# Kernel optimization log

Measured on AMD Instinct MI355X. Metric: run time of the kernel, lower is better.

Reference implementation:

```python
import jax, jax.numpy as jnp
import numpy as np

MARGIN = 0.2
EPS = 1e-5
NEG_SENTINEL = -1e9


def _cos_sim(a, b):
    a = a / jnp.linalg.norm(a, axis=-1, keepdims=True)
    b = b / jnp.linalg.norm(b, axis=-1, keepdims=True)
    return a @ b.T  # [B, B]


def _row_losses(sm, labels):
    # sm: [B, B] similarity matrix; one loop body of the original, vectorized over rows i.
    diag = jnp.diagonal(sm)                      # pos_pair_ (scalar per row)
    pos_valid = diag < (1.0 - EPS)               # pos_pair_[pos_pair_ < 1-eps]
    neg_mask = labels[None, :] != labels[:, None]
    # neg_pair_[neg_pair_ + margin > min(pos_pair_)] ; min of a scalar is itself
    hard = neg_mask & ((sm + MARGIN) > diag[:, None])
    has_neg = jnp.any(hard, axis=1)
    neg_max = jnp.max(jnp.where(hard, sm, NEG_SENTINEL), axis=1)  # max(neg_pair)
    valid = pos_valid & has_neg
    pos_loss = jnp.maximum(0.2 * diag * diag - 0.7 * diag + 0.5, 0.0)
    neg_loss = jnp.maximum(0.9 * neg_max * neg_max - 0.4 * neg_max + 0.03, 0.0)
    return jnp.sum(jnp.where(valid, pos_loss + neg_loss, 0.0))


def setup_inputs() -> dict:
    key = jax.random.key(0)
    k1, k2 = jax.random.split(key)
    B, D = 8192, 256
    audio_embeds = jax.random.normal(k1, (B, D), dtype=jnp.float32)
    text_embeds = jax.random.normal(k2, (B, D), dtype=jnp.float32)
    labels = jnp.arange(B, dtype=jnp.int64)
    return {"audio_embeds": audio_embeds, "text_embeds": text_embeds, "labels": labels}


def reference(audio_embeds, text_embeds, labels):
    scores = _cos_sim(audio_embeds, text_embeds)  # [B, B]
    B = scores.shape[0]
    total = _row_losses(scores, labels) + _row_losses(scores.T, labels)
    return total / B
```

## Files before the change

kernel.cpp:

```cpp
#include <hip/hip_runtime.h>
#include <stdint.h>

#define BM 128
#define BN 128
#define KD 256

typedef __attribute__((ext_vector_type(4))) float f32x4;
typedef __attribute__((ext_vector_type(4))) int   i32x4;
typedef __attribute__((ext_vector_type(8))) int   i32x8;

__device__ __forceinline__ float fmax4(f32x4 v) {
  return fmaxf(fmaxf(v[0], v[1]), fmaxf(v[2], v[3]));
}

__global__ __launch_bounds__(256) void norm_kernel(
    const float* __restrict__ a, const float* __restrict__ b,
    unsigned int* __restrict__ an, unsigned int* __restrict__ bn,
    float* __restrict__ diag, float* __restrict__ out, int D) {
  if (blockIdx.x == 0 && threadIdx.x == 0) out[0] = 0.f;
  const int row = blockIdx.x * 4 + (threadIdx.x >> 6);
  const int l = threadIdx.x & 63;
  const float4 av = ((const float4*)(a + (size_t)row * D))[l];
  const float4 bv = ((const float4*)(b + (size_t)row * D))[l];
  float ssa = av.x*av.x + av.y*av.y + av.z*av.z + av.w*av.w;
  float ssb = bv.x*bv.x + bv.y*bv.y + bv.z*bv.z + bv.w*bv.w;
  float dot = av.x*bv.x + av.y*bv.y + av.z*bv.z + av.w*bv.w;
  for (int off = 1; off < 64; off <<= 1) {
    ssa += __shfl_xor(ssa, off, 64);
    ssb += __shfl_xor(ssb, off, 64);
    dot += __shfl_xor(dot, off, 64);
  }
  const float inva = 1.0f / sqrtf(ssa);
  const float invb = 1.0f / sqrtf(ssb);
  if (l == 0) diag[row] = dot * inva * invb;
  int pa = 0, pb = 0;
  pa = __builtin_amdgcn_cvt_pk_fp8_f32(av.x * inva, av.y * inva, pa, 0);
  pa = __builtin_amdgcn_cvt_pk_fp8_f32(av.z * inva, av.w * inva, pa, 1);
  pb = __builtin_amdgcn_cvt_pk_fp8_f32(bv.x * invb, bv.y * invb, pb, 0);
  pb = __builtin_amdgcn_cvt_pk_fp8_f32(bv.z * invb, bv.w * invb, pb, 1);
  an[(size_t)row * (D / 4) + l] = (unsigned int)pa;
  bn[(size_t)row * (D / 4) + l] = (unsigned int)pb;
}

__global__ __launch_bounds__(256, 2) void gemm_max_kernel(
    const unsigned char* __restrict__ an, const unsigned char* __restrict__ bn,
    const int* __restrict__ labels,
    float* __restrict__ row_part, float* __restrict__ col_part, int B) {
  __shared__ __align__(16) unsigned char sA[BM * KD];
  __shared__ __align__(16) unsigned char sB[BN * KD];
  __shared__ float lds_col[2][BN];

  const int tid  = threadIdx.x;
  const int lane = tid & 63;
  const int w    = tid >> 6;
  const int wm   = w >> 1, wn = w & 1;
  const int tj   = blockIdx.x & 63;
  const int ti   = blockIdx.x >> 6;

  const int sr = lane >> 4;
  const int sc = lane & 15;

  const int fr = lane & 15;
  const int hi = lane >> 4;
  const int p0 = ((2 * hi)     ^ (fr & 7)) * 16;
  const int p1 = ((2 * hi + 1) ^ (fr & 7)) * 16;

  #pragma unroll
  for (int pass = 0; pass < 8; ++pass) {
    const int r0  = pass * 16 + w * 4;
    const int row = r0 + sr;
    const int g = ((sc & 7) ^ (row & 7)) | (sc & 8);
    const unsigned char* ga = an + (size_t)(ti * BM + row) * KD + g * 16;
    const unsigned char* gb = bn + (size_t)(tj * BN + row) * KD + g * 16;
    __builtin_amdgcn_global_load_lds(
        (const __attribute__((address_space(1))) void*)ga,
        (__attribute__((address_space(3))) void*)(sA + r0 * KD + lane * 16), 16, 0, 0);
    __builtin_amdgcn_global_load_lds(
        (const __attribute__((address_space(1))) void*)gb,
        (__attribute__((address_space(3))) void*)(sB + r0 * KD + lane * 16), 16, 0, 0);
  }
  __syncthreads();

  f32x4 acc[4][4];
  #pragma unroll
  for (int mt = 0; mt < 4; ++mt)
    #pragma unroll
    for (int nt = 0; nt < 4; ++nt)
      acc[mt][nt] = (f32x4){0.f, 0.f, 0.f, 0.f};

  const int SC = 0x7F7F7F7F;

  #pragma unroll
  for (int it = 0; it < 2; ++it) {
    i32x8 bf[4];
    #pragma unroll
    for (int nt = 0; nt < 4; ++nt) {
      const unsigned char* rb = sB + (wn * 64 + nt * 16 + fr) * KD + it * 128;
      i32x4 blo = *(const i32x4*)(rb + p0), bhi = *(const i32x4*)(rb + p1);
      bf[nt] = __builtin_shufflevector(blo, bhi, 0, 1, 2, 3, 4, 5, 6, 7);
    }
    #pragma unroll
    for (int mt = 0; mt < 4; ++mt) {
      const unsigned char* ra = sA + (wm * 64 + mt * 16 + fr) * KD + it * 128;
      i32x4 alo = *(const i32x4*)(ra + p0), ahi = *(const i32x4*)(ra + p1);
      i32x8 af = __builtin_shufflevector(alo, ahi, 0, 1, 2, 3, 4, 5, 6, 7);
      #pragma unroll
      for (int nt = 0; nt < 4; ++nt)
        acc[mt][nt] = __builtin_amdgcn_mfma_scale_f32_16x16x128_f8f6f4(
            af, bf[nt], acc[mt][nt], 0, 0, 0, SC, 0, SC);
    }
  }
  __syncthreads();

  int li[4][4], labc[4];
  #pragma unroll
  for (int mt = 0; mt < 4; ++mt)
    #pragma unroll
    for (int r = 0; r < 4; ++r)
      li[mt][r] = labels[ti * BM + wm * 64 + mt * 16 + hi * 4 + r];
  #pragma unroll
  for (int nt = 0; nt < 4; ++nt)
    labc[nt] = labels[tj * BN + wn * 64 + nt * 16 + fr];

  float rp[4][4];
  float cp[4] = {-1e9f, -1e9f, -1e9f, -1e9f};
  #pragma unroll
  for (int mt = 0; mt < 4; ++mt)
    #pragma unroll
    for (int r = 0; r < 4; ++r) {
      const int l0 = li[mt][r];
      float rm = -1e9f;
      #pragma unroll
      for (int nt = 0; nt < 4; ++nt) {
        const float vm = (l0 != labc[nt]) ? acc[mt][nt][r] : -1e9f;
        rm = fmaxf(rm, vm);
        cp[nt] = fmaxf(cp[nt], vm);
      }
      rp[mt][r] = rm;
    }

  float* red = (float*)sA;
  const int s = wn * 16 + fr;
  #pragma unroll
  for (int mt = 0; mt < 4; ++mt)
    #pragma unroll
    for (int r = 0; r < 4; ++r) {
      const int i = wm * 64 + mt * 16 + hi * 4 + r;
      red[i * 32 + (((s >> 2) ^ (i & 7)) << 2) + (s & 3)] = rp[mt][r];
    }

  #pragma unroll
  for (int nt = 0; nt < 4; ++nt) {
    float c = cp[nt];
    c = fmaxf(c, __shfl_xor(c, 16, 64));
    c = fmaxf(c, __shfl_xor(c, 32, 64));
    if (hi == 0) lds_col[wm][wn * 64 + nt * 16 + fr] = c;
  }
  __syncthreads();

  if (tid < BM) {
    const int key = tid & 7;
    const f32x4* rr = (const f32x4*)(red + tid * 32);
    f32x4 m4 = rr[0 ^ key];
    #pragma unroll
    for (int k = 1; k < 8; ++k) {
      f32x4 v = rr[k ^ key];
      m4[0] = fmaxf(m4[0], v[0]); m4[1] = fmaxf(m4[1], v[1]);
      m4[2] = fmaxf(m4[2], v[2]); m4[3] = fmaxf(m4[3], v[3]);
    }
    row_part[(size_t)tj * B + ti * BM + tid] = fmax4(m4);
  } else if (tid < BM + BN) {
    const int t2 = tid - BM;
    col_part[(size_t)ti * B + tj * BN + t2] =
        fmaxf(lds_col[0][t2], lds_col[1][t2]);
  }
}

__global__ __launch_bounds__(256) void finalize_kernel(
    const float* __restrict__ row_part, const float* __restrict__ col_part,
    const float* __restrict__ diag, int B, int T, float* __restrict__ out) {
  const int v = blockIdx.x * 256 + threadIdx.x;
  const bool isrow = v < B;
  const int i = isrow ? v : v - B;
  const float* part = isrow ? row_part : col_part;
  float m = -1e9f;
  for (int t = 0; t < T; ++t) m = fmaxf(m, part[(size_t)t * B + i]);
  const float d = diag[i];
  float loss = 0.f;
  if ((d < 1.0f - 1e-5f) && (m + 0.2f > d)) {
    loss = fmaxf(0.2f * d * d - 0.7f * d + 0.5f, 0.f) +
           fmaxf(0.9f * m * m - 0.4f * m + 0.03f, 0.f);
  }
  for (int off = 1; off < 64; off <<= 1) loss += __shfl_xor(loss, off, 64);
  __shared__ float ssum[4];
  if ((threadIdx.x & 63) == 0) ssum[threadIdx.x >> 6] = loss;
  __syncthreads();
  if (threadIdx.x == 0)
    atomicAdd(out, (ssum[0] + ssum[1] + ssum[2] + ssum[3]) / (float)B);
}

extern "C" void kernel_launch(void* const* d_in, const int* in_sizes, int n_in,
                              void* d_out, int out_size, void* d_ws, size_t ws_size,
                              hipStream_t stream) {
  const float* a      = (const float*)d_in[0];
  const float* b      = (const float*)d_in[1];
  const int*   labels = (const int*)d_in[2];
  const int B = in_sizes[2];
  const int D = in_sizes[0] / B;
  const int T = B / BM;

  char* ws = (char*)d_ws;
  unsigned char* an = (unsigned char*)ws;
  unsigned char* bn = (unsigned char*)(ws + (size_t)B * D);
  float* diag     = (float*)(ws + (size_t)2 * B * D);
  float* row_part = diag + B;
  float* col_part = row_part + (size_t)T * B;

  norm_kernel<<<B / 4, 256, 0, stream>>>(a, b, (unsigned int*)an,
                                         (unsigned int*)bn, diag,
                                         (float*)d_out, D);

  gemm_max_kernel<<<(B / BM) * (B / BN), 256, 0, stream>>>(
      an, bn, labels, row_part, col_part, B);

  finalize_kernel<<<(2 * B) / 256, 256, 0, stream>>>(
      row_part, col_part, diag, B, T, (float*)d_out);
}
```

Before: 123.5 us.

## Make GEMM blocks loop over 16 A tiles with double-buffered LDS prefetch

Each GEMM block now keeps one B column tile resident in LDS and loops over 16 A row tiles. It prefetches the next A tile into a second LDS buffer while computing the current one, with 512 threads arranged as 2x4 waves. The launch drops from 4096 blocks to 256, cutting repeated B loads and per-block setup. Row maxima are reduced with wave shuffles and written straight to global memory per wave column instead of through an LDS reduction. This enlarges the row partial buffer fourfold and makes the finalize pass read many more partials per row, while column partials shrink to four per column.

```diff
diff --git a/kernel.cpp b/kernel.cpp
--- a/kernel.cpp
+++ b/kernel.cpp
@@ -8,10 +8,6 @@
 typedef __attribute__((ext_vector_type(4))) float f32x4;
 typedef __attribute__((ext_vector_type(4))) int   i32x4;
 typedef __attribute__((ext_vector_type(8))) int   i32x8;
-
-__device__ __forceinline__ float fmax4(f32x4 v) {
-  return fmaxf(fmaxf(v[0], v[1]), fmaxf(v[2], v[3]));
-}
 
 __global__ __launch_bounds__(256) void norm_kernel(
     const float* __restrict__ a, const float* __restrict__ b,
@@ -42,20 +38,20 @@
   bn[(size_t)row * (D / 4) + l] = (unsigned int)pb;
 }
 
-__global__ __launch_bounds__(256, 2) void gemm_max_kernel(
+__global__ __launch_bounds__(512, 2) void gemm_max_kernel(
     const unsigned char* __restrict__ an, const unsigned char* __restrict__ bn,
     const int* __restrict__ labels,
     float* __restrict__ row_part, float* __restrict__ col_part, int B) {
-  __shared__ __align__(16) unsigned char sA[BM * KD];
+  __shared__ __align__(16) unsigned char sA[2 * BM * KD];
   __shared__ __align__(16) unsigned char sB[BN * KD];
   __shared__ float lds_col[2][BN];
 
   const int tid  = threadIdx.x;
   const int lane = tid & 63;
   const int w    = tid >> 6;
-  const int wm   = w >> 1, wn = w & 1;
+  const int wm   = w >> 2, wn = w & 3;
+  const int g0   = blockIdx.x >> 6;
   const int tj   = blockIdx.x & 63;
-  const int ti   = blockIdx.x >> 6;
 
   const int sr = lane >> 4;
   const int sc = lane & 15;
@@ -66,123 +62,135 @@
   const int p1 = ((2 * hi + 1) ^ (fr & 7)) * 16;
 
   #pragma unroll
-  for (int pass = 0; pass < 8; ++pass) {
-    const int r0  = pass * 16 + w * 4;
+  for (int pass = 0; pass < 4; ++pass) {
+    const int r0  = pass * 32 + w * 4;
     const int row = r0 + sr;
     const int g = ((sc & 7) ^ (row & 7)) | (sc & 8);
-    const unsigned char* ga = an + (size_t)(ti * BM + row) * KD + g * 16;
     const unsigned char* gb = bn + (size_t)(tj * BN + row) * KD + g * 16;
+    const unsigned char* ga = an + (size_t)(g0 * BM + row) * KD + g * 16;
+    __builtin_amdgcn_global_load_lds(
+        (const __attribute__((address_space(1))) void*)gb,
+        (__attribute__((address_space(3))) void*)(sB + r0 * KD + lane * 16), 16, 0, 0);
     __builtin_amdgcn_global_load_lds(
         (const __attribute__((address_space(1))) void*)ga,
         (__attribute__((address_space(3))) void*)(sA + r0 * KD + lane * 16), 16, 0, 0);
-    __builtin_amdgcn_global_load_lds(
-        (const __attribute__((address_space(1))) void*)gb,
-        (__attribute__((address_space(3))) void*)(sB + r0 * KD + lane * 16), 16, 0, 0);
   }
   __syncthreads();
 
-  f32x4 acc[4][4];
+  int labc[2];
+  labc[0] = labels[tj * BN + wn * 32 + fr];
+  labc[1] = labels[tj * BN + wn * 32 + 16 + fr];
+
+  const int SC = 0x7F7F7F7F;
+  float cp[2] = {-1e9f, -1e9f};
+  int bsel = 0;
+
+  for (int k = 0; k < 16; ++k) {
+    const int ti = g0 + 4 * k;
+
+    if (k < 15) {
+      const int tin = g0 + 4 * (k + 1);
+      #pragma unroll
+      for (int pass = 0; pass < 4; ++pass) {
+        const int r0  = pass * 32 + w * 4;
+        const int row = r0 + sr;
+        const int g = ((sc & 7) ^ (row & 7)) | (sc & 8);
+        const unsigned char* ga = an + (size_t)(tin * BM + row) * KD + g * 16;
+        __builtin_amdgcn_global_load_lds(
+            (const __attribute__((address_space(1))) void*)ga,
+            (__attribute__((address_space(3))) void*)
+                (sA + (bsel ^ 1) * (BM * KD) + r0 * KD + lane * 16), 16, 0, 0);
+      }
+    }
+
+    f32x4 acc[4][2];
+    #pragma unroll
+    for (int mt = 0; mt < 4; ++mt) {
+      acc[mt][0] = (f32x4){0.f, 0.f, 0.f, 0.f};
+      acc[mt][1] = (f32x4){0.f, 0.f, 0.f, 0.f};
+    }
+    const unsigned char* Ab = sA + bsel * (BM * KD);
+    #pragma unroll
+    for (int it = 0; it < 2; ++it) {
+      i32x8 bf[2];
+      #pragma unroll
+      for (int nt = 0; nt < 2; ++nt) {
+        const unsigned char* rb = sB + (wn * 32 + nt * 16 + fr) * KD + it * 128;
+        bf[nt] = __builtin_shufflevector(*(const i32x4*)(rb + p0),
+                                         *(const i32x4*)(rb + p1),
+                                         0, 1, 2, 3, 4, 5, 6, 7);
+      }
+      #pragma unroll
+      for (int mt = 0; mt < 4; ++mt) {
+        const unsigned char* ra = Ab + (wm * 64 + mt * 16 + fr) * KD + it * 128;
+        i32x8 af = __builtin_shufflevector(*(const i32x4*)(ra + p0),
+                                           *(const i32x4*)(ra + p1),
+                                           0, 1, 2, 3, 4, 5, 6, 7);
+        acc[mt][0] = __builtin_amdgcn_mfma_scale_f32_16x16x128_f8f6f4(
+            af, bf[0], acc[mt][0], 0, 0, 0, SC, 0, SC);
+        acc[mt][1] = __builtin_amdgcn_mfma_scale_f32_16x16x128_f8f6f4(
+            af, bf[1], acc[mt][1], 0, 0, 0, SC, 0, SC);
+      }
+    }
+
+    int li[4][4];
+    #pragma unroll
+    for (int mt = 0; mt < 4; ++mt)
+      #pragma unroll
+      for (int r = 0; r < 4; ++r)
+        li[mt][r] = labels[ti * BM + wm * 64 + mt * 16 + hi * 4 + r];
+
+    const size_t rowbase =
+        (size_t)(tj * 4 + wn) * B + (size_t)ti * BM + wm * 64;
+    #pragma unroll
+    for (int mt = 0; mt < 4; ++mt) {
+      float rr4[4];
+      #pragma unroll
+      for (int r = 0; r < 4; ++r) {
+        const int l0 = li[mt][r];
+        const float vm0 = (l0 != labc[0]) ? acc[mt][0][r] : -1e9f;
+        const float vm1 = (l0 != labc[1]) ? acc[mt][1][r] : -1e9f;
+        cp[0] = fmaxf(cp[0], vm0);
+        cp[1] = fmaxf(cp[1], vm1);
+        float rm = fmaxf(vm0, vm1);
+        rm = fmaxf(rm, __shfl_xor(rm, 1, 64));
+        rm = fmaxf(rm, __shfl_xor(rm, 2, 64));
+        rm = fmaxf(rm, __shfl_xor(rm, 4, 64));
+        rm = fmaxf(rm, __shfl_xor(rm, 8, 64));
+        rr4[r] = rm;
+      }
+      if (fr == mt) {
+        f32x4 v = {rr4[0], rr4[1], rr4[2], rr4[3]};
+        *(f32x4*)(row_part + rowbase + mt * 16 + hi * 4) = v;
+      }
+    }
+
+    __syncthreads();
+    bsel ^= 1;
+  }
+
   #pragma unroll
-  for (int mt = 0; mt < 4; ++mt)
-    #pragma unroll
-    for (int nt = 0; nt < 4; ++nt)
-      acc[mt][nt] = (f32x4){0.f, 0.f, 0.f, 0.f};
-
-  const int SC = 0x7F7F7F7F;
-
-  #pragma unroll
-  for (int it = 0; it < 2; ++it) {
-    i32x8 bf[4];
-    #pragma unroll
-    for (int nt = 0; nt < 4; ++nt) {
-      const unsigned char* rb = sB + (wn * 64 + nt * 16 + fr) * KD + it * 128;
-      i32x4 blo = *(const i32x4*)(rb + p0), bhi = *(const i32x4*)(rb + p1);
-      bf[nt] = __builtin_shufflevector(blo, bhi, 0, 1, 2, 3, 4, 5, 6, 7);
-    }
-    #pragma unroll
-    for (int mt = 0; mt < 4; ++mt) {
-      const unsigned char* ra = sA + (wm * 64 + mt * 16 + fr) * KD + it * 128;
-      i32x4 alo = *(const i32x4*)(ra + p0), ahi = *(const i32x4*)(ra + p1);
-      i32x8 af = __builtin_shufflevector(alo, ahi, 0, 1, 2, 3, 4, 5, 6, 7);
-      #pragma unroll
-      for (int nt = 0; nt < 4; ++nt)
-        acc[mt][nt] = __builtin_amdgcn_mfma_scale_f32_16x16x128_f8f6f4(
-            af, bf[nt], acc[mt][nt], 0, 0, 0, SC, 0, SC);
-    }
-  }
-  __syncthreads();
-
-  int li[4][4], labc[4];
-  #pragma unroll
-  for (int mt = 0; mt < 4; ++mt)
-    #pragma unroll
-    for (int r = 0; r < 4; ++r)
-      li[mt][r] = labels[ti * BM + wm * 64 + mt * 16 + hi * 4 + r];
-  #pragma unroll
-  for (int nt = 0; nt < 4; ++nt)
-    labc[nt] = labels[tj * BN + wn * 64 + nt * 16 + fr];
-
-  float rp[4][4];
-  float cp[4] = {-1e9f, -1e9f, -1e9f, -1e9f};
-  #pragma unroll
-  for (int mt = 0; mt < 4; ++mt)
-    #pragma unroll
-    for (int r = 0; r < 4; ++r) {
-      const int l0 = li[mt][r];
-      float rm = -1e9f;
-      #pragma unroll
-      for (int nt = 0; nt < 4; ++nt) {
-        const float vm = (l0 != labc[nt]) ? acc[mt][nt][r] : -1e9f;
-        rm = fmaxf(rm, vm);
-        cp[nt] = fmaxf(cp[nt], vm);
-      }
-      rp[mt][r] = rm;
-    }
-
-  float* red = (float*)sA;
-  const int s = wn * 16 + fr;
-  #pragma unroll
-  for (int mt = 0; mt < 4; ++mt)
-    #pragma unroll
-    for (int r = 0; r < 4; ++r) {
-      const int i = wm * 64 + mt * 16 + hi * 4 + r;
-      red[i * 32 + (((s >> 2) ^ (i & 7)) << 2) + (s & 3)] = rp[mt][r];
-    }
-
-  #pragma unroll
-  for (int nt = 0; nt < 4; ++nt) {
+  for (int nt = 0; nt < 2; ++nt) {
     float c = cp[nt];
     c = fmaxf(c, __shfl_xor(c, 16, 64));
     c = fmaxf(c, __shfl_xor(c, 32, 64));
-    if (hi == 0) lds_col[wm][wn * 64 + nt * 16 + fr] = c;
+    if (hi == 0) lds_col[wm][wn * 32 + nt * 16 + fr] = c;
   }
   __syncthreads();
-
-  if (tid < BM) {
-    const int key = tid & 7;
-    const f32x4* rr = (const f32x4*)(red + tid * 32);
-    f32x4 m4 = rr[0 ^ key];
-    #pragma unroll
-    for (int k = 1; k < 8; ++k) {
-      f32x4 v = rr[k ^ key];
-      m4[0] = fmaxf(m4[0], v[0]); m4[1] = fmaxf(m4[1], v[1]);
-      m4[2] = fmaxf(m4[2], v[2]); m4[3] = fmaxf(m4[3], v[3]);
-    }
-    row_part[(size_t)tj * B + ti * BM + tid] = fmax4(m4);
-  } else if (tid < BM + BN) {
-    const int t2 = tid - BM;
-    col_part[(size_t)ti * B + tj * BN + t2] =
-        fmaxf(lds_col[0][t2], lds_col[1][t2]);
-  }
+  if (tid < BN)
+    col_part[(size_t)g0 * B + tj * BN + tid] =
+        fmaxf(lds_col[0][tid], lds_col[1][tid]);
 }
 
 __global__ __launch_bounds__(256) void finalize_kernel(
     const float* __restrict__ row_part, const float* __restrict__ col_part,
-    const float* __restrict__ diag, int B, int T, float* __restrict__ out) {
+    const float* __restrict__ diag, int B, int Tr, int Tc,
+    float* __restrict__ out) {
   const int v = blockIdx.x * 256 + threadIdx.x;
   const bool isrow = v < B;
   const int i = isrow ? v : v - B;
   const float* part = isrow ? row_part : col_part;
+  const int T = isrow ? Tr : Tc;
   float m = -1e9f;
   for (int t = 0; t < T; ++t) m = fmaxf(m, part[(size_t)t * B + i]);
   const float d = diag[i];
@@ -207,22 +215,23 @@
   const int*   labels = (const int*)d_in[2];
   const int B = in_sizes[2];
   const int D = in_sizes[0] / B;
-  const int T = B / BM;
+  const int Tr = (B / BN) * 4;
+  const int Tc = 4;
 
   char* ws = (char*)d_ws;
   unsigned char* an = (unsigned char*)ws;
   unsigned char* bn = (unsigned char*)(ws + (size_t)B * D);
   float* diag     = (float*)(ws + (size_t)2 * B * D);
   float* row_part = diag + B;
-  float* col_part = row_part + (size_t)T * B;
+  float* col_part = row_part + (size_t)Tr * B;
 
   norm_kernel<<<B / 4, 256, 0, stream>>>(a, b, (unsigned int*)an,
                                          (unsigned int*)bn, diag,
                                          (float*)d_out, D);
 
-  gemm_max_kernel<<<(B / BM) * (B / BN), 256, 0, stream>>>(
+  gemm_max_kernel<<<(B / BM) * (B / BN) / 16, 512, 0, stream>>>(
       an, bn, labels, row_part, col_part, B);
 
   finalize_kernel<<<(2 * B) / 256, 256, 0, stream>>>(
-      row_part, col_part, diag, B, T, (float*)d_out);
-}
+      row_part, col_part, diag, B, Tr, Tc, (float*)d_out);
+}
```

New measurement: 182.1 us. +47.4%, slower.
